# Optimization experiments

Hardware: AMD Instinct MI355X
Metric: run time of the kernel (lower is better)

## Reference

```python
import jax, jax.numpy as jnp
import numpy as np

C = 128
HEAD_CHANNEL = 32
NUM_HEAD = C // HEAD_CHANNEL
SCALE = HEAD_CHANNEL ** 0.5
EPS = 1e-5


def _layernorm(x, g, b):
    mu = jnp.mean(x, axis=-1, keepdims=True)
    var = jnp.mean((x - mu) ** 2, axis=-1, keepdims=True)
    return (x - mu) * jax.lax.rsqrt(var + EPS) * g + b


def _proj(x, g, b, w1, b1, w2, b2):
    # LayerNorm -> Linear(C,2C) -> LeakyReLU(0.01) -> Linear(2C,C); dropout=0 (identity)
    h = jax.nn.leaky_relu(_layernorm(x, g, b) @ w1 + b1, negative_slope=0.01)
    return h @ w2 + b2


def _mlp(x, w1, b1, w2, b2):
    h = jax.nn.leaky_relu(x @ w1 + b1, negative_slope=0.01)
    return h @ w2 + b2


def setup_inputs() -> dict:
    key = jax.random.key(0)
    ks = jax.random.split(key, 32)
    s = 1.0 / np.sqrt(C)
    s2 = 1.0 / np.sqrt(2 * C)
    d = {}
    d["q"] = jax.random.normal(ks[0], (2, C, 64, 64), jnp.float32)
    d["k"] = jax.random.normal(ks[1], (2, C, 64, 64), jnp.float32)
    d["v"] = jax.random.normal(ks[2], (2, C, 64, 64), jnp.float32)
    i = 3
    for p in ("q", "k", "v"):
        d[f"ln_{p}_g"] = jnp.ones((C,), jnp.float32)
        d[f"ln_{p}_b"] = jnp.zeros((C,), jnp.float32)
        d[f"w{p}1"] = jax.random.uniform(ks[i], (C, 2 * C), jnp.float32, -s, s); i += 1
        d[f"b{p}1"] = jnp.zeros((2 * C,), jnp.float32)
        d[f"w{p}2"] = jax.random.uniform(ks[i], (2 * C, C), jnp.float32, -s2, s2); i += 1
        d[f"b{p}2"] = jnp.zeros((C,), jnp.float32)
    for m in ("m1", "m2"):
        d[f"{m}_w1"] = jax.random.uniform(ks[i], (C, 2 * C), jnp.float32, -s, s); i += 1
        d[f"{m}_b1"] = jnp.zeros((2 * C,), jnp.float32)
        d[f"{m}_w2"] = jax.random.uniform(ks[i], (2 * C, C), jnp.float32, -s2, s2); i += 1
        d[f"{m}_b2"] = jnp.zeros((C,), jnp.float32)
    return d


def reference(q, k, v,
              ln_q_g, ln_q_b, wq1, bq1, wq2, bq2,
              ln_k_g, ln_k_b, wk1, bk1, wk2, bk2,
              ln_v_g, ln_v_b, wv1, bv1, wv2, bv2,
              m1_w1, m1_b1, m1_w2, m1_b2,
              m2_w1, m2_b1, m2_w2, m2_b2):
    B, Cc, H, W = q.shape
    S = H * W
    # [B,C,H,W] -> [B,S,C] token layout
    qt = q.transpose(0, 2, 3, 1).reshape(B, S, Cc)
    kt = k.transpose(0, 2, 3, 1).reshape(B, S, Cc)
    vt = v.transpose(0, 2, 3, 1).reshape(B, S, Cc)
    qp = _proj(qt, ln_q_g, ln_q_b, wq1, bq1, wq2, bq2)
    kp = _proj(kt, ln_k_g, ln_k_b, wk1, bk1, wk2, bk2)
    vp = _proj(vt, ln_v_g, ln_v_b, wv1, bv1, wv2, bv2)  # v_attn_1
    qh = qp.reshape(B, S, NUM_HEAD, HEAD_CHANNEL)
    kh = kp.reshape(B, S, NUM_HEAD, HEAD_CHANNEL)
    vh = vp.reshape(B, S, NUM_HEAD, HEAD_CHANNEL)
    attn = jax.nn.softmax(jnp.einsum('bqhd,bkhd->bhqk', qh, kh) / SCALE, axis=-1)
    x = jnp.einsum('bhqk,bkhd->bqhd', attn, vh).reshape(B, S, Cc)
    rs1 = vp + _mlp(x, m1_w1, m1_b1, m1_w2, m1_b2)
    rs2 = rs1 + _mlp(rs1, m2_w1, m2_b1, m2_w2, m2_b2)
    # back to [B,C,H,W]
    return rs2.reshape(B, H, W, Cc).transpose(0, 3, 1, 2)
```

## Files before the change

kernel.cpp:

```cpp
#include <hip/hip_runtime.h>
#include <hip/hip_bf16.h>

typedef __bf16 bf16_t;
typedef __bf16 bf16x2 __attribute__((ext_vector_type(2)));
typedef __bf16 bf16x4 __attribute__((ext_vector_type(4)));
typedef __bf16 bf16x8 __attribute__((ext_vector_type(8)));
typedef float f32x4 __attribute__((ext_vector_type(4)));
typedef float f32x16 __attribute__((ext_vector_type(16)));


static constexpr size_t WS_WPK   = 0;
static constexpr size_t WS_PP    = 655360;
static constexpr size_t WS_VT    = WS_PP + 3ull*2097152;
static constexpr size_t WS_OPART = WS_VT + 2097152;
static constexpr size_t WS_XN    = WS_OPART;
static constexpr size_t WS_LPART = WS_OPART + 8388608;
static constexpr size_t WS_RS1   = WS_LPART + 524288;

struct PrepArgs {
    const float* src[3]; const float* g[3]; const float* bb[3]; bf16_t* dst[3];
    const float* w1[5]; const float* w2[5]; bf16_t* wdst;
};

__global__ __launch_bounds__(256) void prep_kernel(PrepArgs a) {
    __shared__ float xs[64][129];
    __shared__ float mu_s[64], rs_s[64];
    int bx = blockIdx.x;
    if (bx < 384) {
        int z = bx >> 7;
        int t0 = (bx & 127) * 64;
        int b = t0 >> 12;
        int s0 = t0 & 4095;
        const float* src = a.src[z];
        for (int idx = threadIdx.x; idx < 128 * 64; idx += 256) {
            int c = idx >> 6, tx = idx & 63;
            xs[tx][c] = src[(b * 128 + c) * 4096 + s0 + tx];
        }
        __syncthreads();
        {
            int t = threadIdx.x >> 2, jj = threadIdx.x & 3;
            float sum = 0.f, sq = 0.f;
#pragma unroll
            for (int ci = 0; ci < 32; ++ci) {
                float v = xs[t][ci * 4 + jj];
                sum += v; sq += v * v;
            }
            sum += __shfl_xor(sum, 1); sq += __shfl_xor(sq, 1);
            sum += __shfl_xor(sum, 2); sq += __shfl_xor(sq, 2);
            if (jj == 0) {
                float mu = sum * (1.0f / 128.0f);
                float var = sq * (1.0f / 128.0f) - mu * mu;
                mu_s[t] = mu;
                rs_s[t] = rsqrtf(var + 1e-5f);
            }
        }
        __syncthreads();
        const float* g = a.g[z];
        const float* bb = a.bb[z];
        bf16_t* dst = a.dst[z];
        for (int idx = threadIdx.x; idx < 64 * 128; idx += 256) {
            int t = idx >> 7, c = idx & 127;
            float v = (xs[t][c] - mu_s[t]) * rs_s[t] * g[c] + bb[c];
            dst[(t0 + t) * 128 + c] = (bf16_t)v;
        }
    } else {
        float (*ts)[65] = (float(*)[65])xs;
        int wx = bx - 384;
        int p = wx >> 4;
        int t = wx & 15;
        const float* src; int sld, dld, r0, c0; bf16_t* d;
        if (t < 8) {
            src = a.w1[p]; sld = 256; dld = 128;
            r0 = (t >> 2) * 64; c0 = (t & 3) * 64;
            d = a.wdst + p * 65536;
        } else {
            int tt = t - 8;
            src = a.w2[p]; sld = 128; dld = 256;
            r0 = (tt >> 1) * 64; c0 = (tt & 1) * 64;
            d = a.wdst + p * 65536 + 32768;
        }
        for (int i = threadIdx.x; i < 4096; i += 256) {
            int r = i >> 6, c = i & 63;
            ts[r][c] = src[(r0 + r) * sld + c0 + c];
        }
        __syncthreads();
        for (int i = threadIdx.x; i < 4096; i += 256) {
            int c = i >> 6, r = i & 63;
            d[(c0 + c) * dld + (r0 + r)] = (bf16_t)ts[r][c];
        }
    }
}

struct MlpArgs {
    const bf16_t* A[3];
    const bf16_t* W1T[3];
    const float* B1[3];
    const bf16_t* W2T[3];
    const float* B2[3];
    const bf16_t* RESP[3];
    bf16_t* OUT[3];
    bf16_t* VTOUT[3];
    float* FOUT;
};

template <bool RESF, bool FOUTF>
__global__ __launch_bounds__(256) void mlp_kernel(MlpArgs a) {
    __shared__ bf16_t hl[16][264];
    int z = blockIdx.y;
    int w = threadIdx.x >> 6;
    int lane = threadIdx.x & 63;
    int quad = lane >> 4;
    int l15 = lane & 15;
    int m0 = blockIdx.x * 16;

    const bf16_t* arow = a.A[z] + (size_t)(m0 + l15) * 128 + quad * 8;
    bf16x8 af[4];
#pragma unroll
    for (int kt = 0; kt < 4; ++kt) af[kt] = *(const bf16x8*)(arow + kt * 32);

#pragma unroll
    for (int sub = 0; sub < 4; ++sub) {
        int n = w * 64 + sub * 16 + l15;
        const bf16_t* wrow = a.W1T[z] + (size_t)n * 128 + quad * 8;
        f32x4 acc = {0.f, 0.f, 0.f, 0.f};
#pragma unroll
        for (int kt = 0; kt < 4; ++kt) {
            bf16x8 bfrag = *(const bf16x8*)(wrow + kt * 32);
            acc = __builtin_amdgcn_mfma_f32_16x16x32_bf16(af[kt], bfrag, acc, 0, 0, 0);
        }
        float bn = a.B1[z][n];
#pragma unroll
        for (int r = 0; r < 4; ++r) {
            float v = acc[r] + bn;
            v = v > 0.f ? v : 0.01f * v;
            hl[quad * 4 + r][n] = (bf16_t)v;
        }
    }
    __syncthreads();

    bf16x8 hf[8];
#pragma unroll
    for (int kt = 0; kt < 8; ++kt)
        hf[kt] = *(const bf16x8*)(&hl[l15][kt * 32 + quad * 8]);

#pragma unroll
    for (int sub = 0; sub < 2; ++sub) {
        int n = w * 32 + sub * 16 + l15;
        const bf16_t* wrow = a.W2T[z] + (size_t)n * 256 + quad * 8;
        f32x4 acc = {0.f, 0.f, 0.f, 0.f};
#pragma unroll
        for (int kt = 0; kt < 8; ++kt) {
            bf16x8 bfrag = *(const bf16x8*)(wrow + kt * 32);
            acc = __builtin_amdgcn_mfma_f32_16x16x32_bf16(hf[kt], bfrag, acc, 0, 0, 0);
        }
        float bn = a.B2[z][n];
        float vals[4];
#pragma unroll
        for (int r = 0; r < 4; ++r) {
            int m = m0 + quad * 4 + r;
            float v = acc[r] + bn;
            if (RESF) v += (float)a.RESP[z][(size_t)m * 128 + n];
            vals[r] = v;
        }
        if constexpr (FOUTF) {
            int b = m0 >> 12, s0 = m0 & 4095;
            f32x4 ov = {vals[0], vals[1], vals[2], vals[3]};
            *(f32x4*)(a.FOUT + ((size_t)(b * 128 + n)) * 4096 + s0 + quad * 4) = ov;
        } else {
#pragma unroll
            for (int r = 0; r < 4; ++r)
                a.OUT[z][(size_t)(m0 + quad * 4 + r) * 128 + n] = (bf16_t)vals[r];
            if (a.VTOUT[z] != nullptr) {
                int b = m0 >> 12, s0 = m0 & 4095;
                int bh = b * 4 + (n >> 5), d = n & 31;
                bf16x4 tv = {(bf16_t)vals[0], (bf16_t)vals[1], (bf16_t)vals[2], (bf16_t)vals[3]};
                *(bf16x4*)(a.VTOUT[z] + ((size_t)(bh * 32 + d)) * 4096 + s0 + quad * 4) = tv;
            }
        }
    }
}

__global__ __launch_bounds__(256, 2) void attn_kernel(const bf16_t* __restrict__ qp,
                                                      const bf16_t* __restrict__ kp,
                                                      const bf16_t* __restrict__ vt,
                                                      bf16_t* __restrict__ opart,
                                                      float* __restrict__ lpart) {
    int lid = blockIdx.x;
    int bh = lid & 7;
    int r = lid >> 3;
    int split = r & 3;
    int qb = r >> 2;
    int w = threadIdx.x >> 6;
    int lane = threadIdx.x & 63;
    int l31 = lane & 31;
    int h5 = lane >> 5;
    int b = bh >> 2, h = bh & 3;
    int q0 = qb * 256 + w * 64;

    constexpr float kScale = 0.17677669529663687f * 1.4426950408889634f;

    bf16x8 qf[2][2];
#pragma unroll
    for (int s = 0; s < 2; ++s) {
        const bf16_t* qrow = qp + ((size_t)(b * 4096 + q0 + s * 32 + l31)) * 128 + h * 32 + h5 * 8;
        bf16x8 q0r = *(const bf16x8*)(qrow);
        bf16x8 q1r = *(const bf16x8*)(qrow + 16);
#pragma unroll
        for (int j = 0; j < 8; ++j) {
            qf[s][0][j] = (bf16_t)((float)q0r[j] * kScale);
            qf[s][1][j] = (bf16_t)((float)q1r[j] * kScale);
        }
    }

    bf16x8 a_up, a_lo;
    {
        bf16_t one = (bf16_t)1.0f, zer = (bf16_t)0.0f;
#pragma unroll
        for (int j = 0; j < 8; ++j) { a_up[j] = (l31 < 16) ? one : zer; a_lo[j] = (l31 < 16) ? zer : one; }
    }

    int key_m = (l31 & ~12) | ((l31 & 4) << 1) | ((l31 & 8) >> 1);
    const bf16_t* kbase = kp + ((size_t)(b * 4096) + key_m) * 128 + h * 32 + h5 * 8;
    const bf16_t* vbase = vt + ((size_t)(bh * 32) + l31) * 4096 + h5 * 8;

    f32x16 acca = {0.f,0.f,0.f,0.f,0.f,0.f,0.f,0.f,0.f,0.f,0.f,0.f,0.f,0.f,0.f,0.f};
    f32x16 accb = acca, lacc = acca;
    f32x16 zero16 = acca;

    int kt0 = split * 32;
    const bf16_t* kpt = kbase + (size_t)kt0 * 4096;
    const bf16_t* vpt = vbase + kt0 * 32;
    bf16x8 kf0 = *(const bf16x8*)(kpt);
    bf16x8 kf1 = *(const bf16x8*)(kpt + 16);
    bf16x8 vf0 = *(const bf16x8*)(vpt);
    bf16x8 vf1 = *(const bf16x8*)(vpt + 16);

    for (int it = 0; it < 32; ++it) {
        const bf16_t* nkpt = kpt + (it < 31 ? 4096 : 0);
        const bf16_t* nvpt = vpt + (it < 31 ? 32 : 0);
        bf16x8 nk0 = *(const bf16x8*)(nkpt);
        bf16x8 nk1 = *(const bf16x8*)(nkpt + 16);
        bf16x8 nv0 = *(const bf16x8*)(nvpt);
        bf16x8 nv1 = *(const bf16x8*)(nvpt + 16);

        f32x16 sca = __builtin_amdgcn_mfma_f32_32x32x16_bf16(kf0, qf[0][0], zero16, 0, 0, 0);
        sca = __builtin_amdgcn_mfma_f32_32x32x16_bf16(kf1, qf[0][1], sca, 0, 0, 0);
        f32x16 scb = __builtin_amdgcn_mfma_f32_32x32x16_bf16(kf0, qf[1][0], zero16, 0, 0, 0);
        scb = __builtin_amdgcn_mfma_f32_32x32x16_bf16(kf1, qf[1][1], scb, 0, 0, 0);

        bf16x8 pfa0, pfa1, pfb0, pfb1;
#pragma unroll
        for (int j = 0; j < 8; ++j) {
            pfa0[j] = (bf16_t)__builtin_amdgcn_exp2f(sca[j]);
            pfa1[j] = (bf16_t)__builtin_amdgcn_exp2f(sca[8 + j]);
            pfb0[j] = (bf16_t)__builtin_amdgcn_exp2f(scb[j]);
            pfb1[j] = (bf16_t)__builtin_amdgcn_exp2f(scb[8 + j]);
        }

        lacc = __builtin_amdgcn_mfma_f32_32x32x16_bf16(a_up, pfa0, lacc, 0, 0, 0);
        lacc = __builtin_amdgcn_mfma_f32_32x32x16_bf16(a_up, pfa1, lacc, 0, 0, 0);
        lacc = __builtin_amdgcn_mfma_f32_32x32x16_bf16(a_lo, pfb0, lacc, 0, 0, 0);
        lacc = __builtin_amdgcn_mfma_f32_32x32x16_bf16(a_lo, pfb1, lacc, 0, 0, 0);

        acca = __builtin_amdgcn_mfma_f32_32x32x16_bf16(vf0, pfa0, acca, 0, 0, 0);
        acca = __builtin_amdgcn_mfma_f32_32x32x16_bf16(vf1, pfa1, acca, 0, 0, 0);
        accb = __builtin_amdgcn_mfma_f32_32x32x16_bf16(vf0, pfb0, accb, 0, 0, 0);
        accb = __builtin_amdgcn_mfma_f32_32x32x16_bf16(vf1, pfb1, accb, 0, 0, 0);

        kf0 = nk0; kf1 = nk1; vf0 = nv0; vf1 = nv1;
        kpt = nkpt; vpt = nvpt;
    }

    size_t obase0 = ((size_t)(bh * 4 + split) * 4096 + q0 + l31) * 32;
#pragma unroll
    for (int g = 0; g < 4; ++g) {
        bf16x4 ov = {(bf16_t)acca[4*g], (bf16_t)acca[4*g+1], (bf16_t)acca[4*g+2], (bf16_t)acca[4*g+3]};
        *(bf16x4*)(opart + obase0 + 8 * g + 4 * h5) = ov;
    }
    size_t obase1 = obase0 + 32ull * 32;
#pragma unroll
    for (int g = 0; g < 4; ++g) {
        bf16x4 ov = {(bf16_t)accb[4*g], (bf16_t)accb[4*g+1], (bf16_t)accb[4*g+2], (bf16_t)accb[4*g+3]};
        *(bf16x4*)(opart + obase1 + 8 * g + 4 * h5) = ov;
    }
    lpart[(bh * 4 + split) * 4096 + q0 + h5 * 32 + l31] = h5 ? lacc[8] : lacc[0];
}

__global__ __launch_bounds__(256) void mlp1_kernel(const bf16_t* __restrict__ opart,
                                                   const float* __restrict__ lpart,
                                                   const bf16_t* __restrict__ w1t,
                                                   const float* __restrict__ b1,
                                                   const bf16_t* __restrict__ w2t,
                                                   const float* __restrict__ b2,
                                                   const bf16_t* __restrict__ resp,
                                                   bf16_t* __restrict__ outp) {
    __shared__ bf16_t al[16][136];
    __shared__ bf16_t hl[16][264];
    int w = threadIdx.x >> 6;
    int lane = threadIdx.x & 63;
    int quad = lane >> 4;
    int l15 = lane & 15;
    int m0 = blockIdx.x * 16;

    {
        int t = threadIdx.x >> 4;
        int cg = threadIdx.x & 15;
        int m = m0 + t;
        int b = m >> 12, qq = m & 4095;
        int h = cg >> 2, d0 = (cg & 3) * 8;
        int bh = b * 4 + h;
        float accv[8] = {0.f, 0.f, 0.f, 0.f, 0.f, 0.f, 0.f, 0.f};
        float l = 0.f;
#pragma unroll
        for (int s = 0; s < 4; ++s) {
            const bf16_t* op = opart + ((size_t)((bh * 4 + s) * 4096) + qq) * 32 + d0;
            bf16x8 o8 = *(const bf16x8*)op;
#pragma unroll
            for (int j = 0; j < 8; ++j) accv[j] += (float)o8[j];
            l += lpart[(bh * 4 + s) * 4096 + qq];
        }
        float invl = 1.0f / l;
        bf16x8 a8;
#pragma unroll
        for (int j = 0; j < 8; ++j) a8[j] = (bf16_t)(accv[j] * invl);
        *(bf16x8*)(&al[t][cg * 8]) = a8;
    }
    __syncthreads();

    bf16x8 af[4];
#pragma unroll
    for (int kt = 0; kt < 4; ++kt) af[kt] = *(const bf16x8*)(&al[l15][kt * 32 + quad * 8]);

#pragma unroll
    for (int sub = 0; sub < 4; ++sub) {
        int n = w * 64 + sub * 16 + l15;
        const bf16_t* wrow = w1t + (size_t)n * 128 + quad * 8;
        f32x4 acc = {0.f, 0.f, 0.f, 0.f};
#pragma unroll
        for (int kt = 0; kt < 4; ++kt) {
            bf16x8 bfrag = *(const bf16x8*)(wrow + kt * 32);
            acc = __builtin_amdgcn_mfma_f32_16x16x32_bf16(af[kt], bfrag, acc, 0, 0, 0);
        }
        float bn = b1[n];
#pragma unroll
        for (int r = 0; r < 4; ++r) {
            float v = acc[r] + bn;
            v = v > 0.f ? v : 0.01f * v;
            hl[quad * 4 + r][n] = (bf16_t)v;
        }
    }
    __syncthreads();

    bf16x8 hf[8];
#pragma unroll
    for (int kt = 0; kt < 8; ++kt)
        hf[kt] = *(const bf16x8*)(&hl[l15][kt * 32 + quad * 8]);

#pragma unroll
    for (int sub = 0; sub < 2; ++sub) {
        int n = w * 32 + sub * 16 + l15;
        const bf16_t* wrow = w2t + (size_t)n * 256 + quad * 8;
        f32x4 acc = {0.f, 0.f, 0.f, 0.f};
#pragma unroll
        for (int kt = 0; kt < 8; ++kt) {
            bf16x8 bfrag = *(const bf16x8*)(wrow + kt * 32);
            acc = __builtin_amdgcn_mfma_f32_16x16x32_bf16(hf[kt], bfrag, acc, 0, 0, 0);
        }
        float bn = b2[n];
#pragma unroll
        for (int r = 0; r < 4; ++r) {
            int m = m0 + quad * 4 + r;
            float v = acc[r] + bn + (float)resp[(size_t)m * 128 + n];
            outp[(size_t)m * 128 + n] = (bf16_t)v;
        }
    }
}

extern "C" void kernel_launch(void* const* d_in, const int* in_sizes, int n_in,
                              void* d_out, int out_size, void* d_ws, size_t ws_size,
                              hipStream_t stream) {
    const float* q = (const float*)d_in[0];
    const float* k = (const float*)d_in[1];
    const float* v = (const float*)d_in[2];
    const float* ln_g[3] = {(const float*)d_in[3], (const float*)d_in[9], (const float*)d_in[15]};
    const float* ln_b[3] = {(const float*)d_in[4], (const float*)d_in[10], (const float*)d_in[16]};
    const float* w1[5] = {(const float*)d_in[5], (const float*)d_in[11], (const float*)d_in[17],
                          (const float*)d_in[21], (const float*)d_in[25]};
    const float* b1[5] = {(const float*)d_in[6], (const float*)d_in[12], (const float*)d_in[18],
                          (const float*)d_in[22], (const float*)d_in[26]};
    const float* w2[5] = {(const float*)d_in[7], (const float*)d_in[13], (const float*)d_in[19],
                          (const float*)d_in[23], (const float*)d_in[27]};
    const float* b2[5] = {(const float*)d_in[8], (const float*)d_in[14], (const float*)d_in[20],
                          (const float*)d_in[24], (const float*)d_in[28]};
    float* out = (float*)d_out;

    char* ws = (char*)d_ws;
    bf16_t* wpk = (bf16_t*)(ws + WS_WPK);
    bf16_t* pp  = (bf16_t*)(ws + WS_PP);
    bf16_t* vtb = (bf16_t*)(ws + WS_VT);
    bf16_t* xn  = (bf16_t*)(ws + WS_XN);
    bf16_t* opart = (bf16_t*)(ws + WS_OPART);
    float* lpart = (float*)(ws + WS_LPART);
    bf16_t* rs1 = (bf16_t*)(ws + WS_RS1);

    PrepArgs pra;
    pra.src[0] = q; pra.src[1] = k; pra.src[2] = v;
    for (int i = 0; i < 3; ++i) { pra.g[i] = ln_g[i]; pra.bb[i] = ln_b[i]; pra.dst[i] = xn + (size_t)i * 1048576; }
    for (int p = 0; p < 5; ++p) { pra.w1[p] = w1[p]; pra.w2[p] = w2[p]; }
    pra.wdst = wpk;
    prep_kernel<<<464, 256, 0, stream>>>(pra);

    MlpArgs pa;
    for (int p = 0; p < 3; ++p) {
        pa.A[p] = xn + (size_t)p * 1048576;
        pa.W1T[p] = wpk + (size_t)p * 65536; pa.B1[p] = b1[p];
        pa.W2T[p] = wpk + (size_t)p * 65536 + 32768; pa.B2[p] = b2[p];
        pa.RESP[p] = nullptr;
        pa.OUT[p] = pp + (size_t)p * 1048576;
        pa.VTOUT[p] = (p == 2) ? vtb : nullptr;
    }
    pa.FOUT = nullptr;
    mlp_kernel<false, false><<<dim3(512, 3), 256, 0, stream>>>(pa);

    attn_kernel<<<512, 256, 0, stream>>>(pp, pp + 1048576, vtb, opart, lpart);

    mlp1_kernel<<<512, 256, 0, stream>>>(opart, lpart,
                                         wpk + 3ull * 65536, b1[3],
                                         wpk + 3ull * 65536 + 32768, b2[3],
                                         pp + 2ull * 1048576, rs1);

    MlpArgs m2;
    m2.A[0] = rs1; m2.W1T[0] = wpk + 4ull * 65536; m2.B1[0] = b1[4];
    m2.W2T[0] = wpk + 4ull * 65536 + 32768; m2.B2[0] = b2[4];
    m2.RESP[0] = rs1; m2.OUT[0] = nullptr; m2.VTOUT[0] = nullptr; m2.FOUT = out;
    m2.A[1] = m2.A[2] = nullptr; m2.W1T[1] = m2.W1T[2] = nullptr;
    m2.B1[1] = m2.B1[2] = nullptr; m2.W2T[1] = m2.W2T[2] = nullptr;
    m2.B2[1] = m2.B2[2] = nullptr; m2.RESP[1] = m2.RESP[2] = nullptr;
    m2.OUT[1] = m2.OUT[2] = nullptr; m2.VTOUT[1] = m2.VTOUT[2] = nullptr;
    mlp_kernel<true, true><<<dim3(512, 1), 256, 0, stream>>>(m2);
}
```

Measured before the change: 208.0 us.

## Fuse LayerNorm into projection MLP, merge both residual MLPs, double attention KV split

LayerNorm now runs inside the projection kernel, so the normalized bf16 activations are no longer written to and read back from global memory. The two post-attention MLPs are merged into one kernel that keeps rs1 in shared memory and writes the NCHW float output directly. Attention splits the key range 8 ways instead of 4, launching 1024 blocks with a higher occupancy hint, which doubles the partial-output traffic the merge step must reduce. Weight prep becomes its own small kernel, and the launch count drops from five to four.

```diff
diff --git a/kernel.cpp b/kernel.cpp
--- a/kernel.cpp
+++ b/kernel.cpp
@@ -2,7 +2,6 @@
 #include <hip/hip_bf16.h>
 
 typedef __bf16 bf16_t;
-typedef __bf16 bf16x2 __attribute__((ext_vector_type(2)));
 typedef __bf16 bf16x4 __attribute__((ext_vector_type(4)));
 typedef __bf16 bf16x8 __attribute__((ext_vector_type(8)));
 typedef float f32x4 __attribute__((ext_vector_type(4)));
@@ -13,115 +12,95 @@
 static constexpr size_t WS_PP    = 655360;
 static constexpr size_t WS_VT    = WS_PP + 3ull*2097152;
 static constexpr size_t WS_OPART = WS_VT + 2097152;
-static constexpr size_t WS_XN    = WS_OPART;
-static constexpr size_t WS_LPART = WS_OPART + 8388608;
-static constexpr size_t WS_RS1   = WS_LPART + 524288;
-
-struct PrepArgs {
-    const float* src[3]; const float* g[3]; const float* bb[3]; bf16_t* dst[3];
-    const float* w1[5]; const float* w2[5]; bf16_t* wdst;
+static constexpr size_t WS_LPART = WS_OPART + 16777216;
+
+struct WPtrs { const float* w1[5]; const float* w2[5]; };
+
+__global__ __launch_bounds__(256) void prep_weights(WPtrs wp, bf16_t* __restrict__ dst) {
+    __shared__ float ts[64][65];
+    int bx = blockIdx.x;
+    int p = bx >> 4;
+    int t = bx & 15;
+    const float* src; int sld, dld, r0, c0; bf16_t* d;
+    if (t < 8) {
+        src = wp.w1[p]; sld = 256; dld = 128;
+        r0 = (t >> 2) * 64; c0 = (t & 3) * 64;
+        d = dst + p * 65536;
+    } else {
+        int tt = t - 8;
+        src = wp.w2[p]; sld = 128; dld = 256;
+        r0 = (tt >> 1) * 64; c0 = (tt & 1) * 64;
+        d = dst + p * 65536 + 32768;
+    }
+    for (int i = threadIdx.x; i < 4096; i += 256) {
+        int r = i >> 6, c = i & 63;
+        ts[r][c] = src[(r0 + r) * sld + c0 + c];
+    }
+    __syncthreads();
+    for (int i = threadIdx.x; i < 4096; i += 256) {
+        int c = i >> 6, r = i & 63;
+        d[(c0 + c) * dld + (r0 + r)] = (bf16_t)ts[r][c];
+    }
+}
+
+struct ProjArgs {
+    const float* src[3]; const float* g[3]; const float* bb[3];
+    const float* B1[3]; const float* B2[3];
+    bf16_t* OUT[3]; bf16_t* VTOUT;
 };
 
-__global__ __launch_bounds__(256) void prep_kernel(PrepArgs a) {
-    __shared__ float xs[64][129];
-    __shared__ float mu_s[64], rs_s[64];
-    int bx = blockIdx.x;
-    if (bx < 384) {
-        int z = bx >> 7;
-        int t0 = (bx & 127) * 64;
-        int b = t0 >> 12;
-        int s0 = t0 & 4095;
-        const float* src = a.src[z];
-        for (int idx = threadIdx.x; idx < 128 * 64; idx += 256) {
-            int c = idx >> 6, tx = idx & 63;
-            xs[tx][c] = src[(b * 128 + c) * 4096 + s0 + tx];
-        }
-        __syncthreads();
-        {
-            int t = threadIdx.x >> 2, jj = threadIdx.x & 3;
-            float sum = 0.f, sq = 0.f;
-#pragma unroll
-            for (int ci = 0; ci < 32; ++ci) {
-                float v = xs[t][ci * 4 + jj];
-                sum += v; sq += v * v;
-            }
-            sum += __shfl_xor(sum, 1); sq += __shfl_xor(sq, 1);
-            sum += __shfl_xor(sum, 2); sq += __shfl_xor(sq, 2);
-            if (jj == 0) {
-                float mu = sum * (1.0f / 128.0f);
-                float var = sq * (1.0f / 128.0f) - mu * mu;
-                mu_s[t] = mu;
-                rs_s[t] = rsqrtf(var + 1e-5f);
-            }
-        }
-        __syncthreads();
+__global__ __launch_bounds__(256) void projln_kernel(ProjArgs a, const bf16_t* __restrict__ wpk) {
+    __shared__ float xs[16][132];
+    __shared__ bf16_t al[16][136];
+    __shared__ bf16_t hl[16][264];
+    int z = blockIdx.y;
+    int m0 = blockIdx.x * 16;
+    int b = m0 >> 12, s0 = m0 & 4095;
+    int tx = threadIdx.x;
+    int w = tx >> 6;
+    int lane = tx & 63;
+    int quad = lane >> 4;
+    int l15 = lane & 15;
+
+    const float* src = a.src[z];
+    for (int idx = tx; idx < 2048; idx += 256) {
+        int c = idx >> 4, tt = idx & 15;
+        xs[tt][c] = src[(b * 128 + c) * 4096 + s0 + tt];
+    }
+    __syncthreads();
+
+    {
+        int t = tx >> 4, j = tx & 15;
+        float sum = 0.f, sq = 0.f;
+#pragma unroll
+        for (int k = 0; k < 8; ++k) { float v = xs[t][j + 16 * k]; sum += v; sq += v * v; }
+        sum += __shfl_xor(sum, 1); sq += __shfl_xor(sq, 1);
+        sum += __shfl_xor(sum, 2); sq += __shfl_xor(sq, 2);
+        sum += __shfl_xor(sum, 4); sq += __shfl_xor(sq, 4);
+        sum += __shfl_xor(sum, 8); sq += __shfl_xor(sq, 8);
+        float mu = sum * (1.0f / 128.0f);
+        float var = sq * (1.0f / 128.0f) - mu * mu;
+        float rs = rsqrtf(var + 1e-5f);
         const float* g = a.g[z];
         const float* bb = a.bb[z];
-        bf16_t* dst = a.dst[z];
-        for (int idx = threadIdx.x; idx < 64 * 128; idx += 256) {
-            int t = idx >> 7, c = idx & 127;
-            float v = (xs[t][c] - mu_s[t]) * rs_s[t] * g[c] + bb[c];
-            dst[(t0 + t) * 128 + c] = (bf16_t)v;
-        }
-    } else {
-        float (*ts)[65] = (float(*)[65])xs;
-        int wx = bx - 384;
-        int p = wx >> 4;
-        int t = wx & 15;
-        const float* src; int sld, dld, r0, c0; bf16_t* d;
-        if (t < 8) {
-            src = a.w1[p]; sld = 256; dld = 128;
-            r0 = (t >> 2) * 64; c0 = (t & 3) * 64;
-            d = a.wdst + p * 65536;
-        } else {
-            int tt = t - 8;
-            src = a.w2[p]; sld = 128; dld = 256;
-            r0 = (tt >> 1) * 64; c0 = (tt & 1) * 64;
-            d = a.wdst + p * 65536 + 32768;
-        }
-        for (int i = threadIdx.x; i < 4096; i += 256) {
-            int r = i >> 6, c = i & 63;
-            ts[r][c] = src[(r0 + r) * sld + c0 + c];
-        }
-        __syncthreads();
-        for (int i = threadIdx.x; i < 4096; i += 256) {
-            int c = i >> 6, r = i & 63;
-            d[(c0 + c) * dld + (r0 + r)] = (bf16_t)ts[r][c];
-        }
-    }
-}
-
-struct MlpArgs {
-    const bf16_t* A[3];
-    const bf16_t* W1T[3];
-    const float* B1[3];
-    const bf16_t* W2T[3];
-    const float* B2[3];
-    const bf16_t* RESP[3];
-    bf16_t* OUT[3];
-    bf16_t* VTOUT[3];
-    float* FOUT;
-};
-
-template <bool RESF, bool FOUTF>
-__global__ __launch_bounds__(256) void mlp_kernel(MlpArgs a) {
-    __shared__ bf16_t hl[16][264];
-    int z = blockIdx.y;
-    int w = threadIdx.x >> 6;
-    int lane = threadIdx.x & 63;
-    int quad = lane >> 4;
-    int l15 = lane & 15;
-    int m0 = blockIdx.x * 16;
-
-    const bf16_t* arow = a.A[z] + (size_t)(m0 + l15) * 128 + quad * 8;
+#pragma unroll
+        for (int k = 0; k < 8; ++k) {
+            int c = j + 16 * k;
+            al[t][c] = (bf16_t)((xs[t][c] - mu) * rs * g[c] + bb[c]);
+        }
+    }
+    __syncthreads();
+
+    const bf16_t* w1t = wpk + (size_t)z * 65536;
+    const bf16_t* w2t = w1t + 32768;
     bf16x8 af[4];
 #pragma unroll
-    for (int kt = 0; kt < 4; ++kt) af[kt] = *(const bf16x8*)(arow + kt * 32);
+    for (int kt = 0; kt < 4; ++kt) af[kt] = *(const bf16x8*)(&al[l15][kt * 32 + quad * 8]);
 
 #pragma unroll
     for (int sub = 0; sub < 4; ++sub) {
         int n = w * 64 + sub * 16 + l15;
-        const bf16_t* wrow = a.W1T[z] + (size_t)n * 128 + quad * 8;
+        const bf16_t* wrow = w1t + (size_t)n * 128 + quad * 8;
         f32x4 acc = {0.f, 0.f, 0.f, 0.f};
 #pragma unroll
         for (int kt = 0; kt < 4; ++kt) {
@@ -146,7 +125,7 @@
 #pragma unroll
     for (int sub = 0; sub < 2; ++sub) {
         int n = w * 32 + sub * 16 + l15;
-        const bf16_t* wrow = a.W2T[z] + (size_t)n * 256 + quad * 8;
+        const bf16_t* wrow = w2t + (size_t)n * 256 + quad * 8;
         f32x4 acc = {0.f, 0.f, 0.f, 0.f};
 #pragma unroll
         for (int kt = 0; kt < 8; ++kt) {
@@ -156,31 +135,19 @@
         float bn = a.B2[z][n];
         float vals[4];
 #pragma unroll
-        for (int r = 0; r < 4; ++r) {
-            int m = m0 + quad * 4 + r;
-            float v = acc[r] + bn;
-            if (RESF) v += (float)a.RESP[z][(size_t)m * 128 + n];
-            vals[r] = v;
-        }
-        if constexpr (FOUTF) {
-            int b = m0 >> 12, s0 = m0 & 4095;
-            f32x4 ov = {vals[0], vals[1], vals[2], vals[3]};
-            *(f32x4*)(a.FOUT + ((size_t)(b * 128 + n)) * 4096 + s0 + quad * 4) = ov;
-        } else {
-#pragma unroll
-            for (int r = 0; r < 4; ++r)
-                a.OUT[z][(size_t)(m0 + quad * 4 + r) * 128 + n] = (bf16_t)vals[r];
-            if (a.VTOUT[z] != nullptr) {
-                int b = m0 >> 12, s0 = m0 & 4095;
-                int bh = b * 4 + (n >> 5), d = n & 31;
-                bf16x4 tv = {(bf16_t)vals[0], (bf16_t)vals[1], (bf16_t)vals[2], (bf16_t)vals[3]};
-                *(bf16x4*)(a.VTOUT[z] + ((size_t)(bh * 32 + d)) * 4096 + s0 + quad * 4) = tv;
-            }
+        for (int r = 0; r < 4; ++r) vals[r] = acc[r] + bn;
+#pragma unroll
+        for (int r = 0; r < 4; ++r)
+            a.OUT[z][(size_t)(m0 + quad * 4 + r) * 128 + n] = (bf16_t)vals[r];
+        if (z == 2) {
+            int bh = b * 4 + (n >> 5), d = n & 31;
+            bf16x4 tv = {(bf16_t)vals[0], (bf16_t)vals[1], (bf16_t)vals[2], (bf16_t)vals[3]};
+            *(bf16x4*)(a.VTOUT + ((size_t)(bh * 32 + d)) * 4096 + s0 + quad * 4) = tv;
         }
     }
 }
 
-__global__ __launch_bounds__(256, 2) void attn_kernel(const bf16_t* __restrict__ qp,
+__global__ __launch_bounds__(256, 4) void attn_kernel(const bf16_t* __restrict__ qp,
                                                       const bf16_t* __restrict__ kp,
                                                       const bf16_t* __restrict__ vt,
                                                       bf16_t* __restrict__ opart,
@@ -188,8 +155,8 @@
     int lid = blockIdx.x;
     int bh = lid & 7;
     int r = lid >> 3;
-    int split = r & 3;
-    int qb = r >> 2;
+    int split = r & 7;
+    int qb = r >> 3;
     int w = threadIdx.x >> 6;
     int lane = threadIdx.x & 63;
     int l31 = lane & 31;
@@ -227,7 +194,7 @@
     f32x16 accb = acca, lacc = acca;
     f32x16 zero16 = acca;
 
-    int kt0 = split * 32;
+    int kt0 = split * 16;
     const bf16_t* kpt = kbase + (size_t)kt0 * 4096;
     const bf16_t* vpt = vbase + kt0 * 32;
     bf16x8 kf0 = *(const bf16x8*)(kpt);
@@ -235,9 +202,9 @@
     bf16x8 vf0 = *(const bf16x8*)(vpt);
     bf16x8 vf1 = *(const bf16x8*)(vpt + 16);
 
-    for (int it = 0; it < 32; ++it) {
-        const bf16_t* nkpt = kpt + (it < 31 ? 4096 : 0);
-        const bf16_t* nvpt = vpt + (it < 31 ? 32 : 0);
+    for (int it = 0; it < 16; ++it) {
+        const bf16_t* nkpt = kpt + (it < 15 ? 4096 : 0);
+        const bf16_t* nvpt = vpt + (it < 15 ? 32 : 0);
         bf16x8 nk0 = *(const bf16x8*)(nkpt);
         bf16x8 nk1 = *(const bf16x8*)(nkpt + 16);
         bf16x8 nv0 = *(const bf16x8*)(nvpt);
@@ -271,7 +238,7 @@
         kpt = nkpt; vpt = nvpt;
     }
 
-    size_t obase0 = ((size_t)(bh * 4 + split) * 4096 + q0 + l31) * 32;
+    size_t obase0 = ((size_t)(bh * 8 + split) * 4096 + q0 + l31) * 32;
 #pragma unroll
     for (int g = 0; g < 4; ++g) {
         bf16x4 ov = {(bf16_t)acca[4*g], (bf16_t)acca[4*g+1], (bf16_t)acca[4*g+2], (bf16_t)acca[4*g+3]};
@@ -283,41 +250,49 @@
         bf16x4 ov = {(bf16_t)accb[4*g], (bf16_t)accb[4*g+1], (bf16_t)accb[4*g+2], (bf16_t)accb[4*g+3]};
         *(bf16x4*)(opart + obase1 + 8 * g + 4 * h5) = ov;
     }
-    lpart[(bh * 4 + split) * 4096 + q0 + h5 * 32 + l31] = h5 ? lacc[8] : lacc[0];
+    lpart[(bh * 8 + split) * 4096 + q0 + h5 * 32 + l31] = h5 ? lacc[8] : lacc[0];
 }
 
-__global__ __launch_bounds__(256) void mlp1_kernel(const bf16_t* __restrict__ opart,
+__global__ __launch_bounds__(256) void mlpf_kernel(const bf16_t* __restrict__ opart,
                                                    const float* __restrict__ lpart,
-                                                   const bf16_t* __restrict__ w1t,
-                                                   const float* __restrict__ b1,
-                                                   const bf16_t* __restrict__ w2t,
-                                                   const float* __restrict__ b2,
-                                                   const bf16_t* __restrict__ resp,
-                                                   bf16_t* __restrict__ outp) {
+                                                   const bf16_t* __restrict__ wpk,
+                                                   const float* __restrict__ b1a,
+                                                   const float* __restrict__ b2a,
+                                                   const float* __restrict__ b1b,
+                                                   const float* __restrict__ b2b,
+                                                   const bf16_t* __restrict__ vp,
+                                                   float* __restrict__ out) {
     __shared__ bf16_t al[16][136];
+    __shared__ bf16_t al2[16][136];
     __shared__ bf16_t hl[16][264];
     int w = threadIdx.x >> 6;
     int lane = threadIdx.x & 63;
     int quad = lane >> 4;
     int l15 = lane & 15;
     int m0 = blockIdx.x * 16;
+    int bb = m0 >> 12, s0 = m0 & 4095;
+
+    const bf16_t* w1ta = wpk + 3ull * 65536;
+    const bf16_t* w2ta = w1ta + 32768;
+    const bf16_t* w1tb = wpk + 4ull * 65536;
+    const bf16_t* w2tb = w1tb + 32768;
 
     {
         int t = threadIdx.x >> 4;
         int cg = threadIdx.x & 15;
         int m = m0 + t;
-        int b = m >> 12, qq = m & 4095;
+        int qq = m & 4095;
         int h = cg >> 2, d0 = (cg & 3) * 8;
-        int bh = b * 4 + h;
+        int bh = bb * 4 + h;
         float accv[8] = {0.f, 0.f, 0.f, 0.f, 0.f, 0.f, 0.f, 0.f};
         float l = 0.f;
 #pragma unroll
-        for (int s = 0; s < 4; ++s) {
-            const bf16_t* op = opart + ((size_t)((bh * 4 + s) * 4096) + qq) * 32 + d0;
+        for (int s = 0; s < 8; ++s) {
+            const bf16_t* op = opart + ((size_t)((bh * 8 + s) * 4096) + qq) * 32 + d0;
             bf16x8 o8 = *(const bf16x8*)op;
 #pragma unroll
             for (int j = 0; j < 8; ++j) accv[j] += (float)o8[j];
-            l += lpart[(bh * 4 + s) * 4096 + qq];
+            l += lpart[(bh * 8 + s) * 4096 + qq];
         }
         float invl = 1.0f / l;
         bf16x8 a8;
@@ -330,18 +305,17 @@
     bf16x8 af[4];
 #pragma unroll
     for (int kt = 0; kt < 4; ++kt) af[kt] = *(const bf16x8*)(&al[l15][kt * 32 + quad * 8]);
-
 #pragma unroll
     for (int sub = 0; sub < 4; ++sub) {
         int n = w * 64 + sub * 16 + l15;
-        const bf16_t* wrow = w1t + (size_t)n * 128 + quad * 8;
+        const bf16_t* wrow = w1ta + (size_t)n * 128 + quad * 8;
         f32x4 acc = {0.f, 0.f, 0.f, 0.f};
 #pragma unroll
         for (int kt = 0; kt < 4; ++kt) {
             bf16x8 bfrag = *(const bf16x8*)(wrow + kt * 32);
             acc = __builtin_amdgcn_mfma_f32_16x16x32_bf16(af[kt], bfrag, acc, 0, 0, 0);
         }
-        float bn = b1[n];
+        float bn = b1a[n];
 #pragma unroll
         for (int r = 0; r < 4; ++r) {
             float v = acc[r] + bn;
@@ -351,27 +325,76 @@
     }
     __syncthreads();
 
-    bf16x8 hf[8];
-#pragma unroll
-    for (int kt = 0; kt < 8; ++kt)
-        hf[kt] = *(const bf16x8*)(&hl[l15][kt * 32 + quad * 8]);
-
-#pragma unroll
-    for (int sub = 0; sub < 2; ++sub) {
-        int n = w * 32 + sub * 16 + l15;
-        const bf16_t* wrow = w2t + (size_t)n * 256 + quad * 8;
+    {
+        bf16x8 hf[8];
+#pragma unroll
+        for (int kt = 0; kt < 8; ++kt)
+            hf[kt] = *(const bf16x8*)(&hl[l15][kt * 32 + quad * 8]);
+#pragma unroll
+        for (int sub = 0; sub < 2; ++sub) {
+            int n = w * 32 + sub * 16 + l15;
+            const bf16_t* wrow = w2ta + (size_t)n * 256 + quad * 8;
+            f32x4 acc = {0.f, 0.f, 0.f, 0.f};
+#pragma unroll
+            for (int kt = 0; kt < 8; ++kt) {
+                bf16x8 bfrag = *(const bf16x8*)(wrow + kt * 32);
+                acc = __builtin_amdgcn_mfma_f32_16x16x32_bf16(hf[kt], bfrag, acc, 0, 0, 0);
+            }
+            float bn = b2a[n];
+#pragma unroll
+            for (int r = 0; r < 4; ++r) {
+                int m = m0 + quad * 4 + r;
+                float v = acc[r] + bn + (float)vp[(size_t)m * 128 + n];
+                al2[quad * 4 + r][n] = (bf16_t)v;
+            }
+        }
+    }
+    __syncthreads();
+
+    bf16x8 af2[4];
+#pragma unroll
+    for (int kt = 0; kt < 4; ++kt) af2[kt] = *(const bf16x8*)(&al2[l15][kt * 32 + quad * 8]);
+#pragma unroll
+    for (int sub = 0; sub < 4; ++sub) {
+        int n = w * 64 + sub * 16 + l15;
+        const bf16_t* wrow = w1tb + (size_t)n * 128 + quad * 8;
         f32x4 acc = {0.f, 0.f, 0.f, 0.f};
 #pragma unroll
-        for (int kt = 0; kt < 8; ++kt) {
+        for (int kt = 0; kt < 4; ++kt) {
             bf16x8 bfrag = *(const bf16x8*)(wrow + kt * 32);
-            acc = __builtin_amdgcn_mfma_f32_16x16x32_bf16(hf[kt], bfrag, acc, 0, 0, 0);
-        }
-        float bn = b2[n];
+            acc = __builtin_amdgcn_mfma_f32_16x16x32_bf16(af2[kt], bfrag, acc, 0, 0, 0);
+        }
+        float bn = b1b[n];
 #pragma unroll
         for (int r = 0; r < 4; ++r) {
-            int m = m0 + quad * 4 + r;
-            float v = acc[r] + bn + (float)resp[(size_t)m * 128 + n];
-            outp[(size_t)m * 128 + n] = (bf16_t)v;
+            float v = acc[r] + bn;
+            v = v > 0.f ? v : 0.01f * v;
+            hl[quad * 4 + r][n] = (bf16_t)v;
+        }
+    }
+    __syncthreads();
+
+    {
+        bf16x8 hf[8];
+#pragma unroll
+        for (int kt = 0; kt < 8; ++kt)
+            hf[kt] = *(const bf16x8*)(&hl[l15][kt * 32 + quad * 8]);
+#pragma unroll
+        for (int sub = 0; sub < 2; ++sub) {
+            int n = w * 32 + sub * 16 + l15;
+            const bf16_t* wrow = w2tb + (size_t)n * 256 + quad * 8;
+            f32x4 acc = {0.f, 0.f, 0.f, 0.f};
+#pragma unroll
+            for (int kt = 0; kt < 8; ++kt) {
+                bf16x8 bfrag = *(const bf16x8*)(wrow + kt * 32);
+                acc = __builtin_amdgcn_mfma_f32_16x16x32_bf16(hf[kt], bfrag, acc, 0, 0, 0);
+            }
+            float bn = b2b[n];
+            f32x4 ov;
+#pragma unroll
+            for (int r = 0; r < 4; ++r)
+                ov[r] = acc[r] + bn + (float)al2[quad * 4 + r][n];
+            *(f32x4*)(out + ((size_t)(bb * 128 + n)) * 4096 + s0 + quad * 4) = ov;
         }
     }
 }
@@ -398,44 +421,26 @@
     bf16_t* wpk = (bf16_t*)(ws + WS_WPK);
     bf16_t* pp  = (bf16_t*)(ws + WS_PP);
     bf16_t* vtb = (bf16_t*)(ws + WS_VT);
-    bf16_t* xn  = (bf16_t*)(ws + WS_XN);
     bf16_t* opart = (bf16_t*)(ws + WS_OPART);
     float* lpart = (float*)(ws + WS_LPART);
-    bf16_t* rs1 = (bf16_t*)(ws + WS_RS1);
-
-    PrepArgs pra;
-    pra.src[0] = q; pra.src[1] = k; pra.src[2] = v;
-    for (int i = 0; i < 3; ++i) { pra.g[i] = ln_g[i]; pra.bb[i] = ln_b[i]; pra.dst[i] = xn + (size_t)i * 1048576; }
-    for (int p = 0; p < 5; ++p) { pra.w1[p] = w1[p]; pra.w2[p] = w2[p]; }
-    pra.wdst = wpk;
-    prep_kernel<<<464, 256, 0, stream>>>(pra);
-
-    MlpArgs pa;
-    for (int p = 0; p < 3; ++p) {
-        pa.A[p] = xn + (size_t)p * 1048576;
-        pa.W1T[p] = wpk + (size_t)p * 65536; pa.B1[p] = b1[p];
-        pa.W2T[p] = wpk + (size_t)p * 65536 + 32768; pa.B2[p] = b2[p];
-        pa.RESP[p] = nullptr;
-        pa.OUT[p] = pp + (size_t)p * 1048576;
-        pa.VTOUT[p] = (p == 2) ? vtb : nullptr;
-    }
-    pa.FOUT = nullptr;
-    mlp_kernel<false, false><<<dim3(512, 3), 256, 0, stream>>>(pa);
-
-    attn_kernel<<<512, 256, 0, stream>>>(pp, pp + 1048576, vtb, opart, lpart);
-
-    mlp1_kernel<<<512, 256, 0, stream>>>(opart, lpart,
-                                         wpk + 3ull * 65536, b1[3],
-                                         wpk + 3ull * 65536 + 32768, b2[3],
-                                         pp + 2ull * 1048576, rs1);
-
-    MlpArgs m2;
-    m2.A[0] = rs1; m2.W1T[0] = wpk + 4ull * 65536; m2.B1[0] = b1[4];
-    m2.W2T[0] = wpk + 4ull * 65536 + 32768; m2.B2[0] = b2[4];
-    m2.RESP[0] = rs1; m2.OUT[0] = nullptr; m2.VTOUT[0] = nullptr; m2.FOUT = out;
-    m2.A[1] = m2.A[2] = nullptr; m2.W1T[1] = m2.W1T[2] = nullptr;
-    m2.B1[1] = m2.B1[2] = nullptr; m2.W2T[1] = m2.W2T[2] = nullptr;
-    m2.B2[1] = m2.B2[2] = nullptr; m2.RESP[1] = m2.RESP[2] = nullptr;
-    m2.OUT[1] = m2.OUT[2] = nullptr; m2.VTOUT[1] = m2.VTOUT[2] = nullptr;
-    mlp_kernel<true, true><<<dim3(512, 1), 256, 0, stream>>>(m2);
+
+    WPtrs wp;
+    for (int p = 0; p < 5; ++p) { wp.w1[p] = w1[p]; wp.w2[p] = w2[p]; }
+    prep_weights<<<80, 256, 0, stream>>>(wp, wpk);
+
+    ProjArgs pa;
+    pa.src[0] = q; pa.src[1] = k; pa.src[2] = v;
+    for (int i = 0; i < 3; ++i) {
+        pa.g[i] = ln_g[i]; pa.bb[i] = ln_b[i];
+        pa.B1[i] = b1[i]; pa.B2[i] = b2[i];
+        pa.OUT[i] = pp + (size_t)i * 1048576;
+    }
+    pa.VTOUT = vtb;
+    projln_kernel<<<dim3(512, 3), 256, 0, stream>>>(pa, wpk);
+
+    attn_kernel<<<1024, 256, 0, stream>>>(pp, pp + 1048576, vtb, opart, lpart);
+
+    mlpf_kernel<<<512, 256, 0, stream>>>(opart, lpart, wpk,
+                                         b1[3], b2[3], b1[4], b2[4],
+                                         pp + 2ull * 1048576, out);
 }
```

Result: no change. 207.5 us (-0.2%).
